# Performance work log

Measured on AMD Instinct MI355X. Metric: run time of the kernel, lower is better.

The kernel has to match this reference:

```python
import jax, jax.numpy as jnp
import numpy as np

L = 15      # GNN layers
D = 128     # hidden width


def _mlp3(x, w1, b1, w2, b2, w3, b3):
    h = jax.nn.relu(x @ w1 + b1)
    h = jax.nn.relu(h @ w2 + b2)
    return h @ w3 + b3


def _layernorm(x, g, b, eps=1e-5):
    mu = x.mean(-1, keepdims=True)
    var = ((x - mu) ** 2).mean(-1, keepdims=True)
    return (x - mu) / jnp.sqrt(var + eps) * g + b


def _gather(V, idx):
    # V: [B,N,D], idx: [B,E] -> [B,E,D]
    return jax.vmap(lambda v, i: v[i])(V, idx)


def _scatter_sum(e, idx, n):
    # e: [B,E,D], idx: [B,E] -> [B,n,D]
    return jax.vmap(lambda ee, ii: jnp.zeros((n, ee.shape[-1]), ee.dtype).at[ii].add(ee))(e, idx)


def setup_inputs() -> dict:
    key = jax.random.key(0)
    ks = iter(jax.random.split(key, 64))
    B, N, Eg = 1, 10000, 40000

    def lin(fi, fo, pre=()):
        s = 1.0 / np.sqrt(fi)
        w = jax.random.uniform(next(ks), pre + (fi, fo), jnp.float32, -s, s)
        b = jax.random.uniform(next(ks), pre + (fo,), jnp.float32, -s, s)
        return w, b

    inp = {}
    inp['node_pos'] = jax.random.normal(next(ks), (B, N, 3), jnp.float32)
    inp['areas'] = jax.random.uniform(next(ks), (B, N, 1), jnp.float32)
    inp['info'] = jax.random.normal(next(ks), (B, 1, 8), jnp.float32)
    inp['edges'] = jax.random.randint(next(ks), (B, Eg, 2), 0, N, jnp.int32)

    # Encoder MLPs (layer_norm=True)
    for pre, fi in [('fv', 12), ('fe', 4)]:
        w1, b1 = lin(fi, D); w2, b2 = lin(D, D); w3, b3 = lin(D, D)
        inp[pre + '_w1'], inp[pre + '_b1'] = w1, b1
        inp[pre + '_w2'], inp[pre + '_b2'] = w2, b2
        inp[pre + '_w3'], inp[pre + '_b3'] = w3, b3
        inp[pre + '_g'] = jnp.ones((D,), jnp.float32)
        inp[pre + '_bt'] = jnp.zeros((D,), jnp.float32)

    # 15 GNN layers, stacked along leading axis (layer_norm=False)
    for pre, fi in [('ge', D + 2 * D), ('gn', D + D)]:
        w1, b1 = lin(fi, D, (L,)); w2, b2 = lin(D, D, (L,)); w3, b3 = lin(D, D, (L,))
        inp[pre + '_w1'], inp[pre + '_b1'] = w1, b1
        inp[pre + '_w2'], inp[pre + '_b2'] = w2, b2
        inp[pre + '_w3'], inp[pre + '_b3'] = w3, b3

    # Decoder (layer_norm=False, output_size=1)
    w1, b1 = lin(D, D); w2, b2 = lin(D, D); w3, b3 = lin(D, 1)
    inp['de_w1'], inp['de_b1'] = w1, b1
    inp['de_w2'], inp['de_b2'] = w2, b2
    inp['de_w3'], inp['de_b3'] = w3, b3
    return inp


def reference(node_pos, areas, info, edges,
              fv_w1, fv_b1, fv_w2, fv_b2, fv_w3, fv_b3, fv_g, fv_bt,
              fe_w1, fe_b1, fe_w2, fe_b2, fe_w3, fe_b3, fe_g, fe_bt,
              ge_w1, ge_b1, ge_w2, ge_b2, ge_w3, ge_b3,
              gn_w1, gn_b1, gn_w2, gn_b2, gn_w3, gn_b3,
              de_w1, de_b1, de_w2, de_b2, de_w3, de_b3):
    B, N, _ = node_pos.shape
    info_b = jnp.broadcast_to(info, (B, N, info.shape[-1]))
    en_in = jnp.concatenate([node_pos, areas, info_b], -1)  # [B,N,12]

    s, r = edges[..., 0], edges[..., 1]
    dist = _gather(node_pos, s) - _gather(node_pos, r)      # [B,E,3]
    nrm = jnp.sqrt((dist ** 2).sum(-1, keepdims=True))
    E_raw = jnp.concatenate([dist, nrm], -1)                # [B,E,4]

    V = _layernorm(_mlp3(en_in, fv_w1, fv_b1, fv_w2, fv_b2, fv_w3, fv_b3), fv_g, fv_bt)
    E = _layernorm(_mlp3(E_raw, fe_w1, fe_b1, fe_w2, fe_b2, fe_w3, fe_b3), fe_g, fe_bt)

    def step(carry, p):
        V, E = carry
        w1, b1, w2, b2, w3, b3, nw1, nb1, nw2, nb2, nw3, nb3 = p
        e_in = jnp.concatenate([_gather(V, s), _gather(V, r), E], -1)  # [B,E,384]
        e_emb = _mlp3(e_in, w1, b1, w2, b2, w3, b3)
        agg = _scatter_sum(e_emb, s, N)                                # [B,N,128]
        v_emb = _mlp3(jnp.concatenate([V, agg], -1), nw1, nb1, nw2, nb2, nw3, nb3)
        return (V + v_emb, E + e_emb), None

    (V, E), _ = jax.lax.scan(step, (V, E),
                             (ge_w1, ge_b1, ge_w2, ge_b2, ge_w3, ge_b3,
                              gn_w1, gn_b1, gn_w2, gn_b2, gn_w3, gn_b3))

    return _mlp3(V, de_w1, de_b1, de_w2, de_b2, de_w3, de_b3)  # [B,N,1]
```

## Files before the change

kernel.cpp:

```cpp
#include <hip/hip_runtime.h>

#define DD 128
#define N_NODE 10000
#define N_EDGE 40000
#define N_LAYER 15

typedef unsigned short U16;
typedef __attribute__((ext_vector_type(8))) short short8;
typedef __attribute__((ext_vector_type(4))) float f32x4;

enum { A_BF16 = 0, A_EDGE, A_NODE, A_ENCIN, A_ERAW };
enum { EPI_F = 0, EPI_EDGE, EPI_NODE, EPI_DEC };

#define OFF_FV1 0
#define OFF_FV2 4096
#define OFF_FV3 20480
#define OFF_FE1 36864
#define OFF_FE2 40960
#define OFF_FE3 57344
#define OFF_GE1 73728
#define OFF_GE2 811008
#define OFF_GE3 1056768
#define OFF_GN1 1302528
#define OFF_GN2 1794048
#define OFF_GN3 2039808
#define OFF_DE1 2285568
#define OFF_DE2 2301952
#define WT_TOTAL 2318336

static __device__ __forceinline__ U16 f2b(float f) {
    union { float f; unsigned u; } x; x.f = f;
    unsigned u = x.u;
    return (U16)((u + 0x7fffu + ((u >> 16) & 1u)) >> 16);
}
static __device__ __forceinline__ float b2f(U16 u) {
    union { unsigned u; float f; } x; x.u = ((unsigned)u) << 16;
    return x.f;
}

static __device__ __forceinline__ void wgb() {
    __asm__ __volatile__("s_waitcnt lgkmcnt(0)\n\ts_barrier" ::: "memory");
}

__global__ __launch_bounds__(256)
void wprep(const float* fv1, const float* fv2, const float* fv3,
           const float* fe1, const float* fe2, const float* fe3,
           const float* ge1, const float* ge2, const float* ge3,
           const float* gn1, const float* gn2, const float* gn3,
           const float* de1, const float* de2, U16* Wt)
{
    int b = blockIdx.x;
    const float* src; U16* dst; int K, Kpad, k0;
    if      (b < 1)   { src = fv1; K = 12;  Kpad = 32;  dst = Wt + OFF_FV1; k0 = b * 32; }
    else if (b < 5)   { src = fv2; K = 128; Kpad = 128; dst = Wt + OFF_FV2; k0 = (b-1)*32; }
    else if (b < 9)   { src = fv3; K = 128; Kpad = 128; dst = Wt + OFF_FV3; k0 = (b-5)*32; }
    else if (b < 10)  { src = fe1; K = 4;   Kpad = 32;  dst = Wt + OFF_FE1; k0 = (b-9)*32; }
    else if (b < 14)  { src = fe2; K = 128; Kpad = 128; dst = Wt + OFF_FE2; k0 = (b-10)*32; }
    else if (b < 18)  { src = fe3; K = 128; Kpad = 128; dst = Wt + OFF_FE3; k0 = (b-14)*32; }
    else if (b < 198) { int r = b-18,  mi = r/12, s = r%12; src = ge1 + (size_t)mi*384*128; K = 384; Kpad = 384; dst = Wt + OFF_GE1 + (size_t)mi*49152; k0 = s*32; }
    else if (b < 258) { int r = b-198, mi = r/4,  s = r%4;  src = ge2 + (size_t)mi*16384;   K = 128; Kpad = 128; dst = Wt + OFF_GE2 + (size_t)mi*16384; k0 = s*32; }
    else if (b < 318) { int r = b-258, mi = r/4,  s = r%4;  src = ge3 + (size_t)mi*16384;   K = 128; Kpad = 128; dst = Wt + OFF_GE3 + (size_t)mi*16384; k0 = s*32; }
    else if (b < 438) { int r = b-318, mi = r/8,  s = r%8;  src = gn1 + (size_t)mi*32768;   K = 256; Kpad = 256; dst = Wt + OFF_GN1 + (size_t)mi*32768; k0 = s*32; }
    else if (b < 498) { int r = b-438, mi = r/4,  s = r%4;  src = gn2 + (size_t)mi*16384;   K = 128; Kpad = 128; dst = Wt + OFF_GN2 + (size_t)mi*16384; k0 = s*32; }
    else if (b < 558) { int r = b-498, mi = r/4,  s = r%4;  src = gn3 + (size_t)mi*16384;   K = 128; Kpad = 128; dst = Wt + OFF_GN3 + (size_t)mi*16384; k0 = s*32; }
    else if (b < 562) { src = de1; K = 128; Kpad = 128; dst = Wt + OFF_DE1; k0 = (b-558)*32; }
    else              { src = de2; K = 128; Kpad = 128; dst = Wt + OFF_DE2; k0 = (b-562)*32; }

    __shared__ float T[32][129];
    #pragma unroll
    for (int i = 0; i < 16; ++i) {
        int l = threadIdx.x + i * 256;
        int kk = l >> 7, n = l & 127;
        int kg = k0 + kk;
        T[kk][n] = (kg < K) ? src[(size_t)kg * 128 + n] : 0.f;
    }
    __syncthreads();
    int n = threadIdx.x >> 1, h = threadIdx.x & 1;
    union { U16 u[16]; int4 v[2]; } o;
    #pragma unroll
    for (int j = 0; j < 16; ++j) o.u[j] = f2b(T[h * 16 + j][n]);
    int4* d = (int4*)(dst + (size_t)n * Kpad + k0 + h * 16);
    d[0] = o.v[0]; d[1] = o.v[1];
}

__global__ __launch_bounds__(256)
void csr_hist(const int* __restrict__ edges, int* __restrict__ cnt, int Eg)
{
    int e = blockIdx.x * 256 + threadIdx.x;
    if (e < Eg) atomicAdd(&cnt[edges[2 * e]], 1);
}

__global__ __launch_bounds__(256)
void csr_scan(const int* __restrict__ cnt, int* __restrict__ rowptr,
              int* __restrict__ cursor, int n)
{
    __shared__ int ps[256];
    int t = threadIdx.x, base = t * 40;
    int s = 0;
    for (int j = 0; j < 40; ++j) if (base + j < n) s += cnt[base + j];
    ps[t] = s; __syncthreads();
    for (int off = 1; off < 256; off <<= 1) {
        int v = (t >= off) ? ps[t - off] : 0;
        __syncthreads();
        ps[t] += v;
        __syncthreads();
    }
    int run = ps[t] - s;
    for (int j = 0; j < 40; ++j) {
        if (base + j < n) {
            rowptr[base + j] = run;
            cursor[base + j] = run;
            run += cnt[base + j];
        }
    }
    if (t == 255) rowptr[n] = ps[255];
}

__global__ __launch_bounds__(256)
void csr_scatter(const int* __restrict__ edges, int* __restrict__ cursor,
                 int* __restrict__ spos, int Eg)
{
    int e = blockIdx.x * 256 + threadIdx.x;
    if (e < Eg) spos[e] = atomicAdd(&cursor[edges[2 * e]], 1);
}

template<int ASRC, int EPI, int K1, int BM>
__global__ __launch_bounds__(512, 4)
void mlp3(const U16* __restrict__ Af,
          const U16* __restrict__ W1, const float* __restrict__ b1,
          const U16* __restrict__ W2, const float* __restrict__ b2,
          const U16* __restrict__ W3, const float* __restrict__ b3,
          U16* __restrict__ outh, float* __restrict__ outf,
          const int* __restrict__ edges, const int* __restrict__ rowptr,
          const int* __restrict__ spos, float* __restrict__ eEs,
          const U16* __restrict__ Vh, const U16* __restrict__ Ehp,
          const float* __restrict__ pos, const float* __restrict__ area,
          const float* __restrict__ info, const float* __restrict__ w3f,
          int M)
{
    constexpr int NAG = BM / 32;
    __shared__ U16 As[2][BM][40];
    __shared__ U16 Bs[2][128][40];
    __shared__ U16 Hs[BM][132];

    const int tid  = threadIdx.x;
    const int row0 = blockIdx.x * BM;
    const int wave = tid >> 6, lane = tid & 63;
    const int quad = lane >> 4, l16 = lane & 15;
    const int wm = (wave >> 2) * (16 * NAG);
    const int wn = (wave & 3) * 32;
    const int sr = tid >> 2, sh = tid & 3;
    const int br = tid >> 2, bh = tid & 3;
    const int sm = row0 + sr;
    const bool stager = (tid < BM * 4);
    const bool valid  = stager && (sm < M);

    int si = 0, ri = 0, jbeg = 0, jend = 0;
    if ((ASRC == A_EDGE || ASRC == A_ERAW) && valid) {
        si = edges[2 * sm]; ri = edges[2 * sm + 1];
    }
    if (ASRC == A_NODE && valid) { jbeg = rowptr[sm]; jend = rowptr[sm + 1]; }

    f32x4 acc[2][NAG];

    auto zacc = [&] {
        #pragma unroll
        for (int i = 0; i < 2; ++i)
            #pragma unroll
            for (int j = 0; j < NAG; ++j) acc[i][j] = (f32x4)0.f;
    };

    auto ldA = [&](int c) -> int4 {
        if (ASRC == A_ENCIN || ASRC == A_ERAW) {
            union { U16 u[8]; int4 v; } pk;
            #pragma unroll
            for (int j = 0; j < 8; ++j) pk.u[j] = 0;
            if (valid) {
                if (ASRC == A_ENCIN) {
                    #pragma unroll
                    for (int j = 0; j < 8; ++j) {
                        int col = sh * 8 + j;
                        float x = 0.f;
                        if (col < 3)       x = pos[3 * sm + col];
                        else if (col == 3) x = area[sm];
                        else if (col < 12) x = info[col - 4];
                        pk.u[j] = f2b(x);
                    }
                } else if (sh == 0) {
                    float dx = pos[3*si]   - pos[3*ri];
                    float dy = pos[3*si+1] - pos[3*ri+1];
                    float dz = pos[3*si+2] - pos[3*ri+2];
                    float nm = sqrtf(dx*dx + dy*dy + dz*dz);
                    pk.u[0] = f2b(dx); pk.u[1] = f2b(dy);
                    pk.u[2] = f2b(dz); pk.u[3] = f2b(nm);
                }
            }
            return pk.v;
        } else if (ASRC == A_NODE && c >= 4) {
            float a[8];
            #pragma unroll
            for (int i = 0; i < 8; ++i) a[i] = 0.f;
            if (valid) {
                const float* base = eEs + (c - 4) * 32 + sh * 8;
                for (int j = jbeg; j < jend; ++j) {
                    const float4* r = (const float4*)(base + (size_t)j * 128);
                    float4 x0 = r[0], x1 = r[1];
                    a[0]+=x0.x; a[1]+=x0.y; a[2]+=x0.z; a[3]+=x0.w;
                    a[4]+=x1.x; a[5]+=x1.y; a[6]+=x1.z; a[7]+=x1.w;
                }
            }
            union { U16 u[8]; int4 v; } pk;
            #pragma unroll
            for (int i = 0; i < 8; ++i) pk.u[i] = f2b(a[i]);
            return pk.v;
        } else {
            const U16* s;
            if (ASRC == A_BF16)        s = Af + (size_t)sm * K1 + c * 32;
            else if (ASRC == A_EDGE) {
                if (c < 4)             s = Vh  + (size_t)si * 128 + c * 32;
                else if (c < 8)        s = Vh  + (size_t)ri * 128 + (c - 4) * 32;
                else                   s = Ehp + (size_t)sm * 128 + (c - 8) * 32;
            } else                     s = Vh  + (size_t)sm * 128 + c * 32;
            return valid ? *(const int4*)(s + sh * 8) : make_int4(0,0,0,0);
        }
    };

    auto ldW = [&](const U16* W, int Kw, int c) -> int4 {
        const U16* s = W + (size_t)br * Kw + c * 32 + bh * 8;
        return *(const int4*)s;
    };

    auto wrA = [&](int b, int4 v) { if (stager) *(int4*)&As[b][sr][sh * 8] = v; };
    auto wrW = [&](int b, int4 w) { *(int4*)&Bs[b][br][bh * 8] = w; };

    auto mfA = [&](int b) {
        short8 wf[2], af[NAG];
        #pragma unroll
        for (int g = 0; g < 2; ++g)
            wf[g] = *(const short8*)&Bs[b][wn + g*16 + l16][quad * 8];
        #pragma unroll
        for (int g = 0; g < NAG; ++g)
            af[g] = *(const short8*)&As[b][wm + g*16 + l16][quad * 8];
        #pragma unroll
        for (int wg = 0; wg < 2; ++wg)
            #pragma unroll
            for (int ag = 0; ag < NAG; ++ag)
                acc[wg][ag] = __builtin_amdgcn_mfma_f32_16x16x32_bf16(
                    wf[wg], af[ag], acc[wg][ag], 0, 0, 0);
    };

    auto mfH = [&](int c, int b) {
        short8 wf[2], af[NAG];
        #pragma unroll
        for (int g = 0; g < 2; ++g)
            wf[g] = *(const short8*)&Bs[b][wn + g*16 + l16][quad * 8];
        #pragma unroll
        for (int g = 0; g < NAG; ++g)
            af[g] = *(const short8*)&Hs[wm + g*16 + l16][c * 32 + quad * 8];
        #pragma unroll
        for (int wg = 0; wg < 2; ++wg)
            #pragma unroll
            for (int ag = 0; ag < NAG; ++ag)
                acc[wg][ag] = __builtin_amdgcn_mfma_f32_16x16x32_bf16(
                    wf[wg], af[ag], acc[wg][ag], 0, 0, 0);
    };

    auto hwrite = [&](const float* bias) {
        #pragma unroll
        for (int wg = 0; wg < 2; ++wg) {
            f32x4 bv = *(const f32x4*)&bias[wn + wg*16 + quad*4];
            #pragma unroll
            for (int ag = 0; ag < NAG; ++ag) {
                int m  = wm + ag*16 + l16;
                int n0 = wn + wg*16 + quad*4;
                union { U16 u[4]; uint2 q; } pk;
                #pragma unroll
                for (int rg = 0; rg < 4; ++rg)
                    pk.u[rg] = f2b(fmaxf(acc[wg][ag][rg] + bv[rg], 0.f));
                *(uint2*)&Hs[m][n0] = pk.q;
            }
        }
    };

    int4 ra0, ra1, rw0, rw1;
    constexpr int C1 = K1 / 32;

    zacc();
    ra0 = ldA(0); rw0 = ldW(W1, K1, 0);
    if (C1 > 1) { ra1 = ldA(1); rw1 = ldW(W1, K1, 1); }
    wrA(0, ra0); wrW(0, rw0);
    wgb();
    #pragma unroll
    for (int c = 0; c < C1; ++c) {
        if (c + 2 < C1) {
            if ((c & 1) == 0) { ra0 = ldA(c + 2); rw0 = ldW(W1, K1, c + 2); }
            else              { ra1 = ldA(c + 2); rw1 = ldW(W1, K1, c + 2); }
        }
        if (c + 1 < C1) {
            if (((c + 1) & 1) == 0) { wrA(0, ra0); wrW(0, rw0); }
            else                    { wrA(1, ra1); wrW(1, rw1); }
        }
        mfA(c & 1);
        wgb();
    }

    rw0 = ldW(W2, 128, 0); rw1 = ldW(W2, 128, 1);
    hwrite(b1);
    wgb();
    zacc();
    wrW(0, rw0);
    wgb();
    #pragma unroll
    for (int c = 0; c < 4; ++c) {
        if (c + 2 < 4) {
            if ((c & 1) == 0) rw0 = ldW(W2, 128, c + 2);
            else              rw1 = ldW(W2, 128, c + 2);
        }
        if (c + 1 < 4) {
            if (((c + 1) & 1) == 0) wrW(0, rw0);
            else                    wrW(1, rw1);
        }
        mfH(c, c & 1);
        wgb();
    }

    if (EPI == EPI_DEC) {
        hwrite(b2);
        wgb();
        constexpr int TPR = 512 / BM;
        constexpr int CPT = 128 / TPR;
        int r = tid / TPR, s8 = tid % TPR;
        int mg = row0 + r;
        float v = 0.f;
        if (mg < M) {
            const U16* hr = &Hs[r][s8 * CPT];
            const float* wr = w3f + s8 * CPT;
            #pragma unroll
            for (int j = 0; j < CPT; ++j) v += b2f(hr[j]) * wr[j];
        }
        #pragma unroll
        for (int off = 1; off < TPR; off <<= 1) v += __shfl_xor(v, off);
        if (s8 == 0 && mg < M) outf[mg] = v + b3[0];
        return;
    }

    rw0 = ldW(W3, 128, 0); rw1 = ldW(W3, 128, 1);
    hwrite(b2);
    wgb();
    zacc();
    wrW(0, rw0);
    wgb();
    #pragma unroll
    for (int c = 0; c < 4; ++c) {
        if (c + 2 < 4) {
            if ((c & 1) == 0) rw0 = ldW(W3, 128, c + 2);
            else              rw1 = ldW(W3, 128, c + 2);
        }
        if (c + 1 < 4) {
            if (((c + 1) & 1) == 0) wrW(0, rw0);
            else                    wrW(1, rw1);
        }
        mfH(c, c & 1);
        wgb();
    }

    f32x4 bvs[2];
    #pragma unroll
    for (int wg = 0; wg < 2; ++wg)
        bvs[wg] = *(const f32x4*)&b3[wn + wg*16 + quad*4];
    #pragma unroll
    for (int ag = 0; ag < NAG; ++ag) {
        int mg = row0 + wm + ag*16 + l16;
        if (mg >= M) continue;
        int sp = 0;
        if (EPI == EPI_EDGE) sp = spos[mg];
        #pragma unroll
        for (int wg = 0; wg < 2; ++wg) {
            int n0 = wn + wg*16 + quad*4;
            f32x4 v;
            #pragma unroll
            for (int rg = 0; rg < 4; ++rg) v[rg] = acc[wg][ag][rg] + bvs[wg][rg];
            size_t o = (size_t)mg * 128 + n0;
            if (EPI == EPI_F) {
                *(f32x4*)&outf[o] = v;
            } else {
                f32x4 c = *(f32x4*)&outf[o];
                c += v;
                *(f32x4*)&outf[o] = c;
                union { U16 u[4]; uint2 q; } pk;
                #pragma unroll
                for (int rg = 0; rg < 4; ++rg) pk.u[rg] = f2b(c[rg]);
                *(uint2*)&outh[o] = pk.q;
                if (EPI == EPI_EDGE)
                    *(f32x4*)&eEs[(size_t)sp * 128 + n0] = v;
            }
        }
    }
}

__global__ __launch_bounds__(256)
void ln_kernel(float* __restrict__ X, const float* __restrict__ g,
               const float* __restrict__ b, U16* __restrict__ Xh, int rows)
{
    int row  = blockIdx.x * 4 + (threadIdx.x >> 6);
    int lane = threadIdx.x & 63;
    if (row >= rows) return;
    float x0 = X[row * DD + lane];
    float x1 = X[row * DD + 64 + lane];
    float s = x0 + x1, q = x0 * x0 + x1 * x1;
    #pragma unroll
    for (int off = 32; off; off >>= 1) {
        s += __shfl_xor(s, off);
        q += __shfl_xor(q, off);
    }
    float mu  = s * (1.f / 128.f);
    float var = q * (1.f / 128.f) - mu * mu;
    float inv = rsqrtf(var + 1e-5f);
    float y0 = (x0 - mu) * inv * g[lane]      + b[lane];
    float y1 = (x1 - mu) * inv * g[64 + lane] + b[64 + lane];
    X[row * DD + lane]       = y0;
    X[row * DD + 64 + lane]  = y1;
    Xh[row * DD + lane]      = f2b(y0);
    Xh[row * DD + 64 + lane] = f2b(y1);
}

extern "C" void kernel_launch(void* const* d_in, const int* in_sizes, int n_in,
                              void* d_out, int out_size, void* d_ws, size_t ws_size,
                              hipStream_t stream)
{
    (void)in_sizes; (void)n_in; (void)out_size; (void)ws_size;

    const float* pos   = (const float*)d_in[0];
    const float* area  = (const float*)d_in[1];
    const float* info  = (const float*)d_in[2];
    const int*   edges = (const int*)d_in[3];
    const float* fv_w1 = (const float*)d_in[4];
    const float* fv_b1 = (const float*)d_in[5];
    const float* fv_w2 = (const float*)d_in[6];
    const float* fv_b2 = (const float*)d_in[7];
    const float* fv_w3 = (const float*)d_in[8];
    const float* fv_b3 = (const float*)d_in[9];
    const float* fv_g  = (const float*)d_in[10];
    const float* fv_bt = (const float*)d_in[11];
    const float* fe_w1 = (const float*)d_in[12];
    const float* fe_b1 = (const float*)d_in[13];
    const float* fe_w2 = (const float*)d_in[14];
    const float* fe_b2 = (const float*)d_in[15];
    const float* fe_w3 = (const float*)d_in[16];
    const float* fe_b3 = (const float*)d_in[17];
    const float* fe_g  = (const float*)d_in[18];
    const float* fe_bt = (const float*)d_in[19];
    const float* ge_w1 = (const float*)d_in[20];
    const float* ge_b1 = (const float*)d_in[21];
    const float* ge_w2 = (const float*)d_in[22];
    const float* ge_b2 = (const float*)d_in[23];
    const float* ge_w3 = (const float*)d_in[24];
    const float* ge_b3 = (const float*)d_in[25];
    const float* gn_w1 = (const float*)d_in[26];
    const float* gn_b1 = (const float*)d_in[27];
    const float* gn_w2 = (const float*)d_in[28];
    const float* gn_b2 = (const float*)d_in[29];
    const float* gn_w3 = (const float*)d_in[30];
    const float* gn_b3 = (const float*)d_in[31];
    const float* de_w1 = (const float*)d_in[32];
    const float* de_b1 = (const float*)d_in[33];
    const float* de_w2 = (const float*)d_in[34];
    const float* de_b2 = (const float*)d_in[35];
    const float* de_w3 = (const float*)d_in[36];
    const float* de_b3 = (const float*)d_in[37];

    char* p = (char*)d_ws;
    float* Vf   = (float*)p;  p += (size_t)N_NODE * 128 * 4;
    float* Ef   = (float*)p;  p += (size_t)N_EDGE * 128 * 4;
    float* eEs  = (float*)p;  p += (size_t)N_EDGE * 128 * 4;
    U16*  Vh    = (U16*)p;    p += (size_t)N_NODE * 128 * 2;
    U16*  Eh    = (U16*)p;    p += (size_t)N_EDGE * 128 * 2;
    U16*  Wt    = (U16*)p;    p += (size_t)WT_TOTAL * 2;
    int*  rowptr = (int*)p;   p += (size_t)(N_NODE + 4) * 4;
    int*  cursor = (int*)p;   p += (size_t)N_NODE * 4;
    int*  cnt    = (int*)p;   p += (size_t)N_NODE * 4;
    int*  spos   = (int*)p;   p += (size_t)N_EDGE * 4;

    const int gbE   = (N_EDGE + 63) / 64;
    const int gbN32 = (N_NODE + 31) / 32;

    wprep<<<566, 256, 0, stream>>>(fv_w1, fv_w2, fv_w3, fe_w1, fe_w2, fe_w3,
                                   ge_w1, ge_w2, ge_w3, gn_w1, gn_w2, gn_w3,
                                   de_w1, de_w2, Wt);
    hipMemsetAsync(cnt, 0, (size_t)N_NODE * 4, stream);
    csr_hist<<<(N_EDGE + 255) / 256, 256, 0, stream>>>(edges, cnt, N_EDGE);
    csr_scan<<<1, 256, 0, stream>>>(cnt, rowptr, cursor, N_NODE);
    csr_scatter<<<(N_EDGE + 255) / 256, 256, 0, stream>>>(edges, cursor, spos, N_EDGE);

    mlp3<A_ERAW, EPI_F, 32, 64><<<gbE, 512, 0, stream>>>(
        nullptr, Wt + OFF_FE1, fe_b1, Wt + OFF_FE2, fe_b2, Wt + OFF_FE3, fe_b3,
        nullptr, Ef, edges, nullptr, nullptr, nullptr, nullptr, nullptr,
        pos, nullptr, nullptr, nullptr, N_EDGE);
    ln_kernel<<<(N_EDGE + 3) / 4, 256, 0, stream>>>(Ef, fe_g, fe_bt, Eh, N_EDGE);

    mlp3<A_ENCIN, EPI_F, 32, 32><<<gbN32, 512, 0, stream>>>(
        nullptr, Wt + OFF_FV1, fv_b1, Wt + OFF_FV2, fv_b2, Wt + OFF_FV3, fv_b3,
        nullptr, Vf, nullptr, nullptr, nullptr, nullptr, nullptr, nullptr,
        pos, area, info, nullptr, N_NODE);
    ln_kernel<<<(N_NODE + 3) / 4, 256, 0, stream>>>(Vf, fv_g, fv_bt, Vh, N_NODE);

    for (int l = 0; l < N_LAYER; ++l) {
        mlp3<A_EDGE, EPI_EDGE, 384, 64><<<gbE, 512, 0, stream>>>(
            nullptr,
            Wt + OFF_GE1 + (size_t)l * 49152, ge_b1 + (size_t)l * 128,
            Wt + OFF_GE2 + (size_t)l * 16384, ge_b2 + (size_t)l * 128,
            Wt + OFF_GE3 + (size_t)l * 16384, ge_b3 + (size_t)l * 128,
            Eh, Ef, edges, nullptr, spos, eEs, Vh, Eh,
            nullptr, nullptr, nullptr, nullptr, N_EDGE);
        mlp3<A_NODE, EPI_NODE, 256, 32><<<gbN32, 512, 0, stream>>>(
            nullptr,
            Wt + OFF_GN1 + (size_t)l * 32768, gn_b1 + (size_t)l * 128,
            Wt + OFF_GN2 + (size_t)l * 16384, gn_b2 + (size_t)l * 128,
            Wt + OFF_GN3 + (size_t)l * 16384, gn_b3 + (size_t)l * 128,
            Vh, Vf, nullptr, rowptr, nullptr, eEs, Vh, nullptr,
            nullptr, nullptr, nullptr, nullptr, N_NODE);
    }

    mlp3<A_BF16, EPI_DEC, 128, 32><<<gbN32, 512, 0, stream>>>(
        Vh, Wt + OFF_DE1, de_b1, Wt + OFF_DE2, de_b2, nullptr, de_b3,
        nullptr, (float*)d_out, nullptr, nullptr, nullptr, nullptr, nullptr, nullptr,
        nullptr, nullptr, nullptr, de_w3, N_NODE);
}
```

Before: 1.027 ms.

## Fuse encoder layernorm into MLP epilogue and gather edge messages via CSR index

The separate layernorm kernels for the edge and node encoders are removed. Layernorm now runs in the mlp3 epilogue: results are staged in a swizzled shared-memory buffer that aliases the existing tiles, and one wave normalises each row. The edge MLP now writes its messages in edge order, and the node aggregation reads them indirectly through a CSR edge-index list instead of a scatter-position array. This drops two launches and one full read-write pass over the encoder outputs, and makes the edge epilogue stores contiguous. In exchange the per-layer node gather becomes an indirect, less coalesced read, and shared memory is restructured into aliased buffers.

```diff
diff --git a/kernel.cpp b/kernel.cpp
--- a/kernel.cpp
+++ b/kernel.cpp
@@ -1,6 +1,5 @@
 #include <hip/hip_runtime.h>
 
-#define DD 128
 #define N_NODE 10000
 #define N_EDGE 40000
 #define N_LAYER 15
@@ -118,10 +117,10 @@
 
 __global__ __launch_bounds__(256)
 void csr_scatter(const int* __restrict__ edges, int* __restrict__ cursor,
-                 int* __restrict__ spos, int Eg)
+                 int* __restrict__ eidx, int Eg)
 {
     int e = blockIdx.x * 256 + threadIdx.x;
-    if (e < Eg) spos[e] = atomicAdd(&cursor[edges[2 * e]], 1);
+    if (e < Eg) eidx[atomicAdd(&cursor[edges[2 * e]], 1)] = e;
 }
 
 template<int ASRC, int EPI, int K1, int BM>
@@ -132,16 +131,21 @@
           const U16* __restrict__ W3, const float* __restrict__ b3,
           U16* __restrict__ outh, float* __restrict__ outf,
           const int* __restrict__ edges, const int* __restrict__ rowptr,
-          const int* __restrict__ spos, float* __restrict__ eEs,
+          const int* __restrict__ eidx, float* __restrict__ eEs,
           const U16* __restrict__ Vh, const U16* __restrict__ Ehp,
           const float* __restrict__ pos, const float* __restrict__ area,
           const float* __restrict__ info, const float* __restrict__ w3f,
+          const float* __restrict__ lng, const float* __restrict__ lnbp,
           int M)
 {
     constexpr int NAG = BM / 32;
-    __shared__ U16 As[2][BM][40];
-    __shared__ U16 Bs[2][128][40];
-    __shared__ U16 Hs[BM][132];
+    constexpr int BSB = 2 * 128 * 40 * 2;
+    constexpr int PLB = BM * 132 * 2;
+    __shared__ __align__(16) char smem[BSB + PLB];
+    auto Bs  = (U16 (*)[128][40])smem;
+    auto As  = (U16 (*)[BM][40])(smem + BSB);
+    auto Hs  = (U16 (*)[132])(smem + BSB);
+    auto LNb = (float (*)[128])smem;
 
     const int tid  = threadIdx.x;
     const int row0 = blockIdx.x * BM;
@@ -203,7 +207,7 @@
             if (valid) {
                 const float* base = eEs + (c - 4) * 32 + sh * 8;
                 for (int j = jbeg; j < jend; ++j) {
-                    const float4* r = (const float4*)(base + (size_t)j * 128);
+                    const float4* r = (const float4*)(base + (size_t)eidx[j] * 128);
                     float4 x0 = r[0], x1 = r[1];
                     a[0]+=x0.x; a[1]+=x0.y; a[2]+=x0.z; a[3]+=x0.w;
                     a[4]+=x1.x; a[5]+=x1.y; a[6]+=x1.z; a[7]+=x1.w;
@@ -364,6 +368,48 @@
         wgb();
     }
 
+    if (EPI == EPI_F) {
+        #pragma unroll
+        for (int wg = 0; wg < 2; ++wg) {
+            f32x4 bv = *(const f32x4*)&b3[wn + wg*16 + quad*4];
+            #pragma unroll
+            for (int ag = 0; ag < NAG; ++ag) {
+                int m  = wm + ag*16 + l16;
+                int n0 = wn + wg*16 + quad*4;
+                int sw = (m & 7) << 2;
+                #pragma unroll
+                for (int rg = 0; rg < 4; ++rg)
+                    LNb[m][(n0 + rg) ^ sw] = acc[wg][ag][rg] + bv[rg];
+            }
+        }
+        wgb();
+        #pragma unroll
+        for (int r = wave; r < BM; r += 8) {
+            int mg = row0 + r;
+            int sw = (r & 7) << 2;
+            float x0 = LNb[r][lane ^ sw];
+            float x1 = LNb[r][(64 + lane) ^ sw];
+            float s = x0 + x1, q = x0 * x0 + x1 * x1;
+            #pragma unroll
+            for (int off = 32; off; off >>= 1) {
+                s += __shfl_xor(s, off);
+                q += __shfl_xor(q, off);
+            }
+            float mu  = s * (1.f / 128.f);
+            float var = q * (1.f / 128.f) - mu * mu;
+            float inv = rsqrtf(var + 1e-5f);
+            float y0 = (x0 - mu) * inv * lng[lane]      + lnbp[lane];
+            float y1 = (x1 - mu) * inv * lng[64 + lane] + lnbp[64 + lane];
+            if (mg < M) {
+                outf[(size_t)mg * 128 + lane]      = y0;
+                outf[(size_t)mg * 128 + 64 + lane] = y1;
+                outh[(size_t)mg * 128 + lane]      = f2b(y0);
+                outh[(size_t)mg * 128 + 64 + lane] = f2b(y1);
+            }
+        }
+        return;
+    }
+
     f32x4 bvs[2];
     #pragma unroll
     for (int wg = 0; wg < 2; ++wg)
@@ -372,8 +418,6 @@
     for (int ag = 0; ag < NAG; ++ag) {
         int mg = row0 + wm + ag*16 + l16;
         if (mg >= M) continue;
-        int sp = 0;
-        if (EPI == EPI_EDGE) sp = spos[mg];
         #pragma unroll
         for (int wg = 0; wg < 2; ++wg) {
             int n0 = wn + wg*16 + quad*4;
@@ -381,47 +425,17 @@
             #pragma unroll
             for (int rg = 0; rg < 4; ++rg) v[rg] = acc[wg][ag][rg] + bvs[wg][rg];
             size_t o = (size_t)mg * 128 + n0;
-            if (EPI == EPI_F) {
-                *(f32x4*)&outf[o] = v;
-            } else {
-                f32x4 c = *(f32x4*)&outf[o];
-                c += v;
-                *(f32x4*)&outf[o] = c;
-                union { U16 u[4]; uint2 q; } pk;
-                #pragma unroll
-                for (int rg = 0; rg < 4; ++rg) pk.u[rg] = f2b(c[rg]);
-                *(uint2*)&outh[o] = pk.q;
-                if (EPI == EPI_EDGE)
-                    *(f32x4*)&eEs[(size_t)sp * 128 + n0] = v;
-            }
-        }
-    }
-}
-
-__global__ __launch_bounds__(256)
-void ln_kernel(float* __restrict__ X, const float* __restrict__ g,
-               const float* __restrict__ b, U16* __restrict__ Xh, int rows)
-{
-    int row  = blockIdx.x * 4 + (threadIdx.x >> 6);
-    int lane = threadIdx.x & 63;
-    if (row >= rows) return;
-    float x0 = X[row * DD + lane];
-    float x1 = X[row * DD + 64 + lane];
-    float s = x0 + x1, q = x0 * x0 + x1 * x1;
-    #pragma unroll
-    for (int off = 32; off; off >>= 1) {
-        s += __shfl_xor(s, off);
-        q += __shfl_xor(q, off);
-    }
-    float mu  = s * (1.f / 128.f);
-    float var = q * (1.f / 128.f) - mu * mu;
-    float inv = rsqrtf(var + 1e-5f);
-    float y0 = (x0 - mu) * inv * g[lane]      + b[lane];
-    float y1 = (x1 - mu) * inv * g[64 + lane] + b[64 + lane];
-    X[row * DD + lane]       = y0;
-    X[row * DD + 64 + lane]  = y1;
-    Xh[row * DD + lane]      = f2b(y0);
-    Xh[row * DD + 64 + lane] = f2b(y1);
+            f32x4 c = *(f32x4*)&outf[o];
+            c += v;
+            *(f32x4*)&outf[o] = c;
+            union { U16 u[4]; uint2 q; } pk;
+            #pragma unroll
+            for (int rg = 0; rg < 4; ++rg) pk.u[rg] = f2b(c[rg]);
+            *(uint2*)&outh[o] = pk.q;
+            if (EPI == EPI_EDGE)
+                *(f32x4*)&eEs[o] = v;
+        }
+    }
 }
 
 extern "C" void kernel_launch(void* const* d_in, const int* in_sizes, int n_in,
@@ -479,7 +493,7 @@
     int*  rowptr = (int*)p;   p += (size_t)(N_NODE + 4) * 4;
     int*  cursor = (int*)p;   p += (size_t)N_NODE * 4;
     int*  cnt    = (int*)p;   p += (size_t)N_NODE * 4;
-    int*  spos   = (int*)p;   p += (size_t)N_EDGE * 4;
+    int*  eidx   = (int*)p;   p += (size_t)N_EDGE * 4;
 
     const int gbE   = (N_EDGE + 63) / 64;
     const int gbN32 = (N_NODE + 31) / 32;
@@ -490,19 +504,17 @@
     hipMemsetAsync(cnt, 0, (size_t)N_NODE * 4, stream);
     csr_hist<<<(N_EDGE + 255) / 256, 256, 0, stream>>>(edges, cnt, N_EDGE);
     csr_scan<<<1, 256, 0, stream>>>(cnt, rowptr, cursor, N_NODE);
-    csr_scatter<<<(N_EDGE + 255) / 256, 256, 0, stream>>>(edges, cursor, spos, N_EDGE);
+    csr_scatter<<<(N_EDGE + 255) / 256, 256, 0, stream>>>(edges, cursor, eidx, N_EDGE);
 
     mlp3<A_ERAW, EPI_F, 32, 64><<<gbE, 512, 0, stream>>>(
         nullptr, Wt + OFF_FE1, fe_b1, Wt + OFF_FE2, fe_b2, Wt + OFF_FE3, fe_b3,
-        nullptr, Ef, edges, nullptr, nullptr, nullptr, nullptr, nullptr,
-        pos, nullptr, nullptr, nullptr, N_EDGE);
-    ln_kernel<<<(N_EDGE + 3) / 4, 256, 0, stream>>>(Ef, fe_g, fe_bt, Eh, N_EDGE);
+        Eh, Ef, edges, nullptr, nullptr, nullptr, nullptr, nullptr,
+        pos, nullptr, nullptr, nullptr, fe_g, fe_bt, N_EDGE);
 
     mlp3<A_ENCIN, EPI_F, 32, 32><<<gbN32, 512, 0, stream>>>(
         nullptr, Wt + OFF_FV1, fv_b1, Wt + OFF_FV2, fv_b2, Wt + OFF_FV3, fv_b3,
-        nullptr, Vf, nullptr, nullptr, nullptr, nullptr, nullptr, nullptr,
-        pos, area, info, nullptr, N_NODE);
-    ln_kernel<<<(N_NODE + 3) / 4, 256, 0, stream>>>(Vf, fv_g, fv_bt, Vh, N_NODE);
+        Vh, Vf, nullptr, nullptr, nullptr, nullptr, nullptr, nullptr,
+        pos, area, info, nullptr, fv_g, fv_bt, N_NODE);
 
     for (int l = 0; l < N_LAYER; ++l) {
         mlp3<A_EDGE, EPI_EDGE, 384, 64><<<gbE, 512, 0, stream>>>(
@@ -510,19 +522,19 @@
             Wt + OFF_GE1 + (size_t)l * 49152, ge_b1 + (size_t)l * 128,
             Wt + OFF_GE2 + (size_t)l * 16384, ge_b2 + (size_t)l * 128,
             Wt + OFF_GE3 + (size_t)l * 16384, ge_b3 + (size_t)l * 128,
-            Eh, Ef, edges, nullptr, spos, eEs, Vh, Eh,
-            nullptr, nullptr, nullptr, nullptr, N_EDGE);
+            Eh, Ef, edges, nullptr, nullptr, eEs, Vh, Eh,
+            nullptr, nullptr, nullptr, nullptr, nullptr, nullptr, N_EDGE);
         mlp3<A_NODE, EPI_NODE, 256, 32><<<gbN32, 512, 0, stream>>>(
             nullptr,
             Wt + OFF_GN1 + (size_t)l * 32768, gn_b1 + (size_t)l * 128,
             Wt + OFF_GN2 + (size_t)l * 16384, gn_b2 + (size_t)l * 128,
             Wt + OFF_GN3 + (size_t)l * 16384, gn_b3 + (size_t)l * 128,
-            Vh, Vf, nullptr, rowptr, nullptr, eEs, Vh, nullptr,
-            nullptr, nullptr, nullptr, nullptr, N_NODE);
+            Vh, Vf, nullptr, rowptr, eidx, eEs, Vh, nullptr,
+            nullptr, nullptr, nullptr, nullptr, nullptr, nullptr, N_NODE);
     }
 
     mlp3<A_BF16, EPI_DEC, 128, 32><<<gbN32, 512, 0, stream>>>(
         Vh, Wt + OFF_DE1, de_b1, Wt + OFF_DE2, de_b2, nullptr, de_b3,
         nullptr, (float*)d_out, nullptr, nullptr, nullptr, nullptr, nullptr, nullptr,
-        nullptr, nullptr, nullptr, de_w3, N_NODE);
-}
+        nullptr, nullptr, nullptr, de_w3, nullptr, nullptr, N_NODE);
+}
```

Measured after the change: 1.280 ms. +24.6%, slower.

## Widen MLP K-chunks to 64 and alias A and H tiles in shared memory

Applied to the files above, without the earlier changes.

The fused three-layer MLP kernel now stages K in 64-wide chunks instead of 32, which halves the number of barrier-separated pipeline steps per layer. Layers 2 and 3 each become two double-buffered steps. The A staging tile and the hidden-activation tile now share one LDS pool, keeping shared memory roughly constant despite the larger tiles, and the K=32 encoder path gets its own special case. The aim is fewer synchronisations and larger loads per step, at the cost of more registers per thread and tighter ordering requirements on the shared pool.

```diff
diff --git a/kernel.cpp b/kernel.cpp
--- a/kernel.cpp
+++ b/kernel.cpp
@@ -41,6 +41,8 @@
 static __device__ __forceinline__ void wgb() {
     __asm__ __volatile__("s_waitcnt lgkmcnt(0)\n\ts_barrier" ::: "memory");
 }
+
+struct I4x2 { int4 a, b; };
 
 __global__ __launch_bounds__(256)
 void wprep(const float* fv1, const float* fv2, const float* fv3,
@@ -139,9 +141,13 @@
           int M)
 {
     constexpr int NAG = BM / 32;
-    __shared__ U16 As[2][BM][40];
-    __shared__ U16 Bs[2][128][40];
-    __shared__ U16 Hs[BM][132];
+    __shared__ U16 Bs[2][128][72];
+    constexpr int ASB = 2 * BM * 68 * 2;
+    constexpr int HSB = BM * 132 * 2;
+    constexpr int PLB = (ASB > HSB) ? ASB : HSB;
+    __shared__ __align__(16) char pool[PLB];
+    auto As = (U16 (*)[BM][68])pool;
+    auto Hs = (U16 (*)[132])pool;
 
     const int tid  = threadIdx.x;
     const int row0 = blockIdx.x * BM;
@@ -149,17 +155,20 @@
     const int quad = lane >> 4, l16 = lane & 15;
     const int wm = (wave >> 2) * (16 * NAG);
     const int wn = (wave & 3) * 32;
-    const int sr = tid >> 2, sh = tid & 3;
-    const int br = tid >> 2, bh = tid & 3;
-    const int sm = row0 + sr;
-    const bool stager = (tid < BM * 4);
-    const bool valid  = stager && (sm < M);
+    const int sr8 = tid >> 3, sh8 = tid & 7;
+    const int sm8 = row0 + sr8;
+    const bool stg8 = (tid < BM * 8);
+    const bool val8 = stg8 && (sm8 < M);
+    const int sr4 = tid >> 2, sh4 = tid & 3;
+    const int sm4 = row0 + sr4;
+    const bool stg4 = (tid < BM * 4);
+    const bool val4 = stg4 && (sm4 < M);
+    const int brw = tid >> 2, bhw = tid & 3;
 
     int si = 0, ri = 0, jbeg = 0, jend = 0;
-    if ((ASRC == A_EDGE || ASRC == A_ERAW) && valid) {
-        si = edges[2 * sm]; ri = edges[2 * sm + 1];
-    }
-    if (ASRC == A_NODE && valid) { jbeg = rowptr[sm]; jend = rowptr[sm + 1]; }
+    if (ASRC == A_EDGE && val8) { si = edges[2 * sm8]; ri = edges[2 * sm8 + 1]; }
+    if (ASRC == A_ERAW && val4) { si = edges[2 * sm4]; ri = edges[2 * sm4 + 1]; }
+    if (ASRC == A_NODE && val8) { jbeg = rowptr[sm8]; jend = rowptr[sm8 + 1]; }
 
     f32x4 acc[2][NAG];
 
@@ -170,38 +179,14 @@
             for (int j = 0; j < NAG; ++j) acc[i][j] = (f32x4)0.f;
     };
 
-    auto ldA = [&](int c) -> int4 {
-        if (ASRC == A_ENCIN || ASRC == A_ERAW) {
-            union { U16 u[8]; int4 v; } pk;
-            #pragma unroll
-            for (int j = 0; j < 8; ++j) pk.u[j] = 0;
-            if (valid) {
-                if (ASRC == A_ENCIN) {
-                    #pragma unroll
-                    for (int j = 0; j < 8; ++j) {
-                        int col = sh * 8 + j;
-                        float x = 0.f;
-                        if (col < 3)       x = pos[3 * sm + col];
-                        else if (col == 3) x = area[sm];
-                        else if (col < 12) x = info[col - 4];
-                        pk.u[j] = f2b(x);
-                    }
-                } else if (sh == 0) {
-                    float dx = pos[3*si]   - pos[3*ri];
-                    float dy = pos[3*si+1] - pos[3*ri+1];
-                    float dz = pos[3*si+2] - pos[3*ri+2];
-                    float nm = sqrtf(dx*dx + dy*dy + dz*dz);
-                    pk.u[0] = f2b(dx); pk.u[1] = f2b(dy);
-                    pk.u[2] = f2b(dz); pk.u[3] = f2b(nm);
-                }
-            }
-            return pk.v;
-        } else if (ASRC == A_NODE && c >= 4) {
+    auto ldA64 = [&](int c) -> int4 {
+        int kk = c * 64 + sh8 * 8;
+        if (ASRC == A_NODE && kk >= 128) {
             float a[8];
             #pragma unroll
             for (int i = 0; i < 8; ++i) a[i] = 0.f;
-            if (valid) {
-                const float* base = eEs + (c - 4) * 32 + sh * 8;
+            if (val8) {
+                const float* base = eEs + (kk - 128);
                 for (int j = jbeg; j < jend; ++j) {
                     const float4* r = (const float4*)(base + (size_t)j * 128);
                     float4 x0 = r[0], x1 = r[1];
@@ -215,54 +200,95 @@
             return pk.v;
         } else {
             const U16* s;
-            if (ASRC == A_BF16)        s = Af + (size_t)sm * K1 + c * 32;
+            if (ASRC == A_BF16)        s = Af + (size_t)sm8 * K1 + kk;
             else if (ASRC == A_EDGE) {
-                if (c < 4)             s = Vh  + (size_t)si * 128 + c * 32;
-                else if (c < 8)        s = Vh  + (size_t)ri * 128 + (c - 4) * 32;
-                else                   s = Ehp + (size_t)sm * 128 + (c - 8) * 32;
-            } else                     s = Vh  + (size_t)sm * 128 + c * 32;
-            return valid ? *(const int4*)(s + sh * 8) : make_int4(0,0,0,0);
-        }
-    };
-
-    auto ldW = [&](const U16* W, int Kw, int c) -> int4 {
-        const U16* s = W + (size_t)br * Kw + c * 32 + bh * 8;
-        return *(const int4*)s;
-    };
-
-    auto wrA = [&](int b, int4 v) { if (stager) *(int4*)&As[b][sr][sh * 8] = v; };
-    auto wrW = [&](int b, int4 w) { *(int4*)&Bs[b][br][bh * 8] = w; };
-
-    auto mfA = [&](int b) {
-        short8 wf[2], af[NAG];
-        #pragma unroll
-        for (int g = 0; g < 2; ++g)
-            wf[g] = *(const short8*)&Bs[b][wn + g*16 + l16][quad * 8];
-        #pragma unroll
-        for (int g = 0; g < NAG; ++g)
-            af[g] = *(const short8*)&As[b][wm + g*16 + l16][quad * 8];
-        #pragma unroll
-        for (int wg = 0; wg < 2; ++wg)
-            #pragma unroll
-            for (int ag = 0; ag < NAG; ++ag)
-                acc[wg][ag] = __builtin_amdgcn_mfma_f32_16x16x32_bf16(
-                    wf[wg], af[ag], acc[wg][ag], 0, 0, 0);
+                if (kk < 128)      s = Vh  + (size_t)si  * 128 + kk;
+                else if (kk < 256) s = Vh  + (size_t)ri  * 128 + (kk - 128);
+                else               s = Ehp + (size_t)sm8 * 128 + (kk - 256);
+            } else                     s = Vh  + (size_t)sm8 * 128 + kk;
+            return val8 ? *(const int4*)s : make_int4(0, 0, 0, 0);
+        }
+    };
+
+    auto ldW64 = [&](const U16* W, int Kw, int c) -> I4x2 {
+        const U16* s = W + (size_t)brw * Kw + c * 64 + bhw * 16;
+        I4x2 r;
+        r.a = ((const int4*)s)[0];
+        r.b = ((const int4*)s)[1];
+        return r;
+    };
+
+    auto wrA64 = [&](int b, int4 v) { if (stg8) *(int4*)&As[b][sr8][sh8 * 8] = v; };
+    auto wrW64 = [&](int b, I4x2 w) {
+        *(int4*)&Bs[b][brw][bhw * 16]     = w.a;
+        *(int4*)&Bs[b][brw][bhw * 16 + 8] = w.b;
+    };
+
+    auto ldA32 = [&]() -> int4 {
+        union { U16 u[8]; int4 v; } pk;
+        #pragma unroll
+        for (int j = 0; j < 8; ++j) pk.u[j] = 0;
+        if (val4) {
+            if (ASRC == A_ENCIN) {
+                #pragma unroll
+                for (int j = 0; j < 8; ++j) {
+                    int col = sh4 * 8 + j;
+                    float x = 0.f;
+                    if (col < 3)       x = pos[3 * sm4 + col];
+                    else if (col == 3) x = area[sm4];
+                    else if (col < 12) x = info[col - 4];
+                    pk.u[j] = f2b(x);
+                }
+            } else if (sh4 == 0) {
+                float dx = pos[3*si]   - pos[3*ri];
+                float dy = pos[3*si+1] - pos[3*ri+1];
+                float dz = pos[3*si+2] - pos[3*ri+2];
+                float nm = sqrtf(dx*dx + dy*dy + dz*dz);
+                pk.u[0] = f2b(dx); pk.u[1] = f2b(dy);
+                pk.u[2] = f2b(dz); pk.u[3] = f2b(nm);
+            }
+        }
+        return pk.v;
+    };
+    auto ldW32 = [&](const U16* W) -> int4 {
+        return *(const int4*)(W + (size_t)brw * 32 + bhw * 8);
+    };
+
+    auto mfA = [&](int b, int nks) {
+        for (int ks = 0; ks < nks; ++ks) {
+            short8 wf[2], af[NAG];
+            #pragma unroll
+            for (int g = 0; g < 2; ++g)
+                wf[g] = *(const short8*)&Bs[b][wn + g*16 + l16][ks * 32 + quad * 8];
+            #pragma unroll
+            for (int g = 0; g < NAG; ++g)
+                af[g] = *(const short8*)&As[b][wm + g*16 + l16][ks * 32 + quad * 8];
+            #pragma unroll
+            for (int wg = 0; wg < 2; ++wg)
+                #pragma unroll
+                for (int ag = 0; ag < NAG; ++ag)
+                    acc[wg][ag] = __builtin_amdgcn_mfma_f32_16x16x32_bf16(
+                        wf[wg], af[ag], acc[wg][ag], 0, 0, 0);
+        }
     };
 
     auto mfH = [&](int c, int b) {
-        short8 wf[2], af[NAG];
-        #pragma unroll
-        for (int g = 0; g < 2; ++g)
-            wf[g] = *(const short8*)&Bs[b][wn + g*16 + l16][quad * 8];
-        #pragma unroll
-        for (int g = 0; g < NAG; ++g)
-            af[g] = *(const short8*)&Hs[wm + g*16 + l16][c * 32 + quad * 8];
-        #pragma unroll
-        for (int wg = 0; wg < 2; ++wg)
-            #pragma unroll
-            for (int ag = 0; ag < NAG; ++ag)
-                acc[wg][ag] = __builtin_amdgcn_mfma_f32_16x16x32_bf16(
-                    wf[wg], af[ag], acc[wg][ag], 0, 0, 0);
+        #pragma unroll
+        for (int ks = 0; ks < 2; ++ks) {
+            short8 wf[2], af[NAG];
+            #pragma unroll
+            for (int g = 0; g < 2; ++g)
+                wf[g] = *(const short8*)&Bs[b][wn + g*16 + l16][ks * 32 + quad * 8];
+            #pragma unroll
+            for (int g = 0; g < NAG; ++g)
+                af[g] = *(const short8*)&Hs[wm + g*16 + l16][c * 64 + ks * 32 + quad * 8];
+            #pragma unroll
+            for (int wg = 0; wg < 2; ++wg)
+                #pragma unroll
+                for (int ag = 0; ag < NAG; ++ag)
+                    acc[wg][ag] = __builtin_amdgcn_mfma_f32_16x16x32_bf16(
+                        wf[wg], af[ag], acc[wg][ag], 0, 0, 0);
+        }
     };
 
     auto hwrite = [&](const float* bias) {
@@ -282,45 +308,48 @@
         }
     };
 
-    int4 ra0, ra1, rw0, rw1;
-    constexpr int C1 = K1 / 32;
-
     zacc();
-    ra0 = ldA(0); rw0 = ldW(W1, K1, 0);
-    if (C1 > 1) { ra1 = ldA(1); rw1 = ldW(W1, K1, 1); }
-    wrA(0, ra0); wrW(0, rw0);
-    wgb();
-    #pragma unroll
-    for (int c = 0; c < C1; ++c) {
-        if (c + 2 < C1) {
-            if ((c & 1) == 0) { ra0 = ldA(c + 2); rw0 = ldW(W1, K1, c + 2); }
-            else              { ra1 = ldA(c + 2); rw1 = ldW(W1, K1, c + 2); }
-        }
-        if (c + 1 < C1) {
-            if (((c + 1) & 1) == 0) { wrA(0, ra0); wrW(0, rw0); }
-            else                    { wrA(1, ra1); wrW(1, rw1); }
-        }
-        mfA(c & 1);
-        wgb();
-    }
-
-    rw0 = ldW(W2, 128, 0); rw1 = ldW(W2, 128, 1);
-    hwrite(b1);
-    wgb();
-    zacc();
-    wrW(0, rw0);
-    wgb();
-    #pragma unroll
-    for (int c = 0; c < 4; ++c) {
-        if (c + 2 < 4) {
-            if ((c & 1) == 0) rw0 = ldW(W2, 128, c + 2);
-            else              rw1 = ldW(W2, 128, c + 2);
-        }
-        if (c + 1 < 4) {
-            if (((c + 1) & 1) == 0) wrW(0, rw0);
-            else                    wrW(1, rw1);
-        }
-        mfH(c, c & 1);
+    if constexpr (K1 == 32) {
+        wrA64(0, make_int4(0,0,0,0));
+        if (stg4) *(int4*)&As[0][sr4][sh4 * 8] = ldA32();
+        wrW64(0, I4x2{make_int4(0,0,0,0), make_int4(0,0,0,0)});
+        *(int4*)&Bs[0][brw][bhw * 8] = ldW32(W1);
+        wgb();
+        mfA(0, 1);
+        wgb();
+    } else {
+        constexpr int C1 = K1 / 64;
+        int4 ra0, ra1; I4x2 rw0, rw1;
+        ra0 = ldA64(0); rw0 = ldW64(W1, K1, 0);
+        if (C1 > 1) { ra1 = ldA64(1); rw1 = ldW64(W1, K1, 1); }
+        wrA64(0, ra0); wrW64(0, rw0);
+        wgb();
+        #pragma unroll
+        for (int c = 0; c < C1; ++c) {
+            if (c + 2 < C1) {
+                if ((c & 1) == 0) { ra0 = ldA64(c + 2); rw0 = ldW64(W1, K1, c + 2); }
+                else              { ra1 = ldA64(c + 2); rw1 = ldW64(W1, K1, c + 2); }
+            }
+            if (c + 1 < C1) {
+                if (((c + 1) & 1) == 0) { wrA64(0, ra0); wrW64(0, rw0); }
+                else                    { wrA64(1, ra1); wrW64(1, rw1); }
+            }
+            mfA(c & 1, 2);
+            wgb();
+        }
+    }
+
+    {
+        I4x2 rw0 = ldW64(W2, 128, 0), rw1 = ldW64(W2, 128, 1);
+        hwrite(b1);
+        wgb();
+        zacc();
+        wrW64(0, rw0);
+        wgb();
+        wrW64(1, rw1);
+        mfH(0, 0);
+        wgb();
+        mfH(1, 1);
         wgb();
     }
 
@@ -344,24 +373,17 @@
         return;
     }
 
-    rw0 = ldW(W3, 128, 0); rw1 = ldW(W3, 128, 1);
-    hwrite(b2);
-    wgb();
-    zacc();
-    wrW(0, rw0);
-    wgb();
-    #pragma unroll
-    for (int c = 0; c < 4; ++c) {
-        if (c + 2 < 4) {
-            if ((c & 1) == 0) rw0 = ldW(W3, 128, c + 2);
-            else              rw1 = ldW(W3, 128, c + 2);
-        }
-        if (c + 1 < 4) {
-            if (((c + 1) & 1) == 0) wrW(0, rw0);
-            else                    wrW(1, rw1);
-        }
-        mfH(c, c & 1);
-        wgb();
+    {
+        I4x2 rw0 = ldW64(W3, 128, 0), rw1 = ldW64(W3, 128, 1);
+        hwrite(b2);
+        wgb();
+        zacc();
+        wrW64(0, rw0);
+        wgb();
+        wrW64(1, rw1);
+        mfH(0, 0);
+        wgb();
+        mfH(1, 1);
     }
 
     f32x4 bvs[2];
@@ -481,8 +503,8 @@
     int*  cnt    = (int*)p;   p += (size_t)N_NODE * 4;
     int*  spos   = (int*)p;   p += (size_t)N_EDGE * 4;
 
-    const int gbE   = (N_EDGE + 63) / 64;
-    const int gbN32 = (N_NODE + 31) / 32;
+    const int gbE = (N_EDGE + 63) / 64;
+    const int gbN = (N_NODE + 31) / 32;
 
     wprep<<<566, 256, 0, stream>>>(fv_w1, fv_w2, fv_w3, fe_w1, fe_w2, fe_w3,
                                    ge_w1, ge_w2, ge_w3, gn_w1, gn_w2, gn_w3,
@@ -498,7 +520,7 @@
         pos, nullptr, nullptr, nullptr, N_EDGE);
     ln_kernel<<<(N_EDGE + 3) / 4, 256, 0, stream>>>(Ef, fe_g, fe_bt, Eh, N_EDGE);
 
-    mlp3<A_ENCIN, EPI_F, 32, 32><<<gbN32, 512, 0, stream>>>(
+    mlp3<A_ENCIN, EPI_F, 32, 32><<<gbN, 512, 0, stream>>>(
         nullptr, Wt + OFF_FV1, fv_b1, Wt + OFF_FV2, fv_b2, Wt + OFF_FV3, fv_b3,
         nullptr, Vf, nullptr, nullptr, nullptr, nullptr, nullptr, nullptr,
         pos, area, info, nullptr, N_NODE);
@@ -512,7 +534,7 @@
             Wt + OFF_GE3 + (size_t)l * 16384, ge_b3 + (size_t)l * 128,
             Eh, Ef, edges, nullptr, spos, eEs, Vh, Eh,
             nullptr, nullptr, nullptr, nullptr, N_EDGE);
-        mlp3<A_NODE, EPI_NODE, 256, 32><<<gbN32, 512, 0, stream>>>(
+        mlp3<A_NODE, EPI_NODE, 256, 32><<<gbN, 512, 0, stream>>>(
             nullptr,
             Wt + OFF_GN1 + (size_t)l * 32768, gn_b1 + (size_t)l * 128,
             Wt + OFF_GN2 + (size_t)l * 16384, gn_b2 + (size_t)l * 128,
@@ -521,7 +543,7 @@
             nullptr, nullptr, nullptr, nullptr, N_NODE);
     }
 
-    mlp3<A_BF16, EPI_DEC, 128, 32><<<gbN32, 512, 0, stream>>>(
+    mlp3<A_BF16, EPI_DEC, 128, 32><<<gbN, 512, 0, stream>>>(
         Vh, Wt + OFF_DE1, de_b1, Wt + OFF_DE2, de_b2, nullptr, de_b3,
         nullptr, (float*)d_out, nullptr, nullptr, nullptr, nullptr, nullptr, nullptr,
         nullptr, nullptr, nullptr, de_w3, N_NODE);
```

New measurement: 1.267 ms. 1.23x slower.
